# Performance work log

Hardware: AMD Instinct MI355X
Metric: run time of the kernel (lower is better)

## Reference

```python
import jax, jax.numpy as jnp
import numpy as np

EPS = 1e-12

def _l2norm(x):
    # F.normalize(p=2, dim=-1) semantics: x / max(||x||, eps)
    n = jnp.sqrt(jnp.sum(x * x, axis=-1, keepdims=True))
    return x / jnp.maximum(n, EPS)

def _split_heads(x, h):
    b, l, d = x.shape
    return x.reshape(b, l, h, d // h).transpose(0, 2, 1, 3)  # (B,H,L,dh)

def _join_heads(x):
    b, h, l, dh = x.shape
    return x.transpose(0, 2, 1, 3).reshape(b, l, h * dh)

def setup_inputs() -> dict:
    key = jax.random.key(0)
    B, L, D = 4, 4096, 1024
    ks = jax.random.split(key, 12)
    s = 1.0 / np.sqrt(D)
    inp = {
        "queries": jax.random.normal(ks[0], (B, L, D), jnp.float32),
        "values": jax.random.normal(ks[1], (B, L, D), jnp.float32),
        "keys": jax.random.normal(ks[2], (B, L, D), jnp.float32),
        "key_attention_mask": jnp.ones((B, L), jnp.float32),
        "Wq": jax.random.uniform(ks[3], (D, D), jnp.float32, -s, s),
        "bq": jax.random.uniform(ks[4], (D,), jnp.float32, -s, s),
        "Wk": jax.random.uniform(ks[5], (D, D), jnp.float32, -s, s),
        "bk": jax.random.uniform(ks[6], (D,), jnp.float32, -s, s),
        "Wv": jax.random.uniform(ks[7], (D, D), jnp.float32, -s, s),
        "bv": jax.random.uniform(ks[8], (D,), jnp.float32, -s, s),
        "Wo": jax.random.uniform(ks[9], (D, D), jnp.float32, -s, s),
        "bo": jax.random.uniform(ks[10], (D,), jnp.float32, -s, s),
    }
    return inp

def reference(queries, values, keys, key_attention_mask, Wq, bq, Wk, bk, Wv, bv, Wo, bo):
    nhead = 16
    L2 = keys.shape[1]
    qp = jnp.einsum('bld,ed->ble', queries, Wq) + bq
    kp = jnp.einsum('bld,ed->ble', keys, Wk) + bk
    vp = jnp.einsum('bld,ed->ble', values, Wv) + bv
    Q = _split_heads(qp, nhead)   # (B,H,L1,dh)
    K = _split_heads(kp, nhead)   # (B,H,L2,dh)
    V = _split_heads(vp, nhead)   # (B,H,L2,dh)
    V_minus = jnp.minimum(V, 0.0)
    V_plus = jnp.maximum(V, 0.0)
    Q = jax.nn.sigmoid(Q)
    scaled_K = jax.nn.sigmoid(K) / L2
    # AmplitudeEmbedding: L2-normalize feature maps along feature dim
    Q = _l2norm(Q)
    scaled_K = _l2norm(scaled_K)
    kv_plus = jnp.einsum('bhld,bhlc,bl->bhdc', scaled_K, V_plus, key_attention_mask)
    heads_plus = _l2norm(jnp.einsum('bhld,bhdc->bhlc', Q, kv_plus))
    kv_minus = jnp.einsum('bhld,bhlc,bl->bhdc', scaled_K, V_minus, key_attention_mask)
    heads_minus = _l2norm(jnp.einsum('bhld,bhdc->bhlc', Q, kv_minus))
    out = _join_heads(heads_plus + heads_minus)  # (B,L1,D)
    return jnp.einsum('blc,dc->bld', out, Wo) + bo
```

## Files before the change

### kernel.cpp

```cpp
#include <hip/hip_runtime.h>
#include <stdint.h>

#define B_  4
#define L_  4096
#define D_  1024
#define H_  16
#define DH  64
#define M_  (B_*L_)

typedef _Float16 f16;
typedef __attribute__((ext_vector_type(8))) _Float16 f16x8;
typedef __attribute__((ext_vector_type(4))) _Float16 f16x4;
typedef __attribute__((ext_vector_type(4))) float    f32x4;

__device__ __forceinline__ void cp16(const void* g, void* l) {
  __builtin_amdgcn_global_load_lds(
      (const __attribute__((address_space(1))) void*)g,
      (__attribute__((address_space(3))) void*)l,
      16, 0, 0);
}

#define MFMA(a,b,c) __builtin_amdgcn_mfma_f32_16x16x32_f16(a,b,c,0,0,0)

#define PH_IN do { __builtin_amdgcn_s_barrier(); \
  asm volatile("s_waitcnt lgkmcnt(0)" ::: "memory"); \
  __builtin_amdgcn_sched_barrier(0); \
  __builtin_amdgcn_s_setprio(1); } while (0)
#define PH_OUT do { __builtin_amdgcn_s_setprio(0); \
  __builtin_amdgcn_sched_barrier(0); \
  asm volatile("" ::: "memory"); \
  __builtin_amdgcn_s_barrier(); } while (0)
#define PH_OUT_VM(nimm) do { __builtin_amdgcn_s_setprio(0); \
  __builtin_amdgcn_sched_barrier(0); \
  asm volatile("s_waitcnt vmcnt(" #nimm ")" ::: "memory"); \
  __builtin_amdgcn_s_barrier(); } while (0)

__global__ __launch_bounds__(256) void k_cvt_f16(const float* __restrict__ x,
                                                 f16* __restrict__ y, int n8) {
  int i = blockIdx.x * 256 + threadIdx.x;
  if (i >= n8) return;
  const float4* xv = (const float4*)x;
  float4 a = xv[2*i], b = xv[2*i+1];
  f16x8 o;
  o[0]=(f16)a.x; o[1]=(f16)a.y; o[2]=(f16)a.z; o[3]=(f16)a.w;
  o[4]=(f16)b.x; o[5]=(f16)b.y; o[6]=(f16)b.z; o[7]=(f16)b.w;
  ((f16x8*)y)[i] = o;
}

__global__ __launch_bounds__(256) void k_cvt2(const float* __restrict__ x0,
                                              f16* __restrict__ y0,
                                              const float* __restrict__ x1,
                                              f16* __restrict__ y1, int n8each) {
  int i = blockIdx.x * 256 + threadIdx.x;
  const float* x = x0; f16* y = y0;
  if (i >= n8each) { x = x1; y = y1; i -= n8each; }
  const float4* xv = (const float4*)x;
  float4 a = xv[2*i], b = xv[2*i+1];
  f16x8 o;
  o[0]=(f16)a.x; o[1]=(f16)a.y; o[2]=(f16)a.z; o[3]=(f16)a.w;
  o[4]=(f16)b.x; o[5]=(f16)b.y; o[6]=(f16)b.z; o[7]=(f16)b.w;
  ((f16x8*)y)[i] = o;
}

__device__ __forceinline__ void split_one(const float* __restrict__ x,
                                          f16* __restrict__ cat, int i) {
  float4 a = ((const float4*)x)[i];
  int n  = i >> 8;
  int k4 = i & 255;
  f16 h0=(f16)a.x, h1=(f16)a.y, h2=(f16)a.z, h3=(f16)a.w;
  f16x4 hv = {h0, h1, h2, h3};
  f16x4 lv = {(f16)(a.x-(float)h0), (f16)(a.y-(float)h1),
              (f16)(a.z-(float)h2), (f16)(a.w-(float)h3)};
  size_t rh = (size_t)((n >> 4) * 32 + (n & 15));
  ((f16x4*)cat)[rh * 256 + k4]        = hv;
  ((f16x4*)cat)[(rh + 16) * 256 + k4] = lv;
}

__global__ __launch_bounds__(256) void k_split2(const float* __restrict__ x0,
                                                f16* __restrict__ c0,
                                                const float* __restrict__ x1,
                                                f16* __restrict__ c1, int n4each) {
  int i = blockIdx.x * 256 + threadIdx.x;
  if (i < n4each) split_one(x0, c0, i);
  else            split_one(x1, c1, i - n4each);
}

struct GemmJob {
  const f16* A; const f16* Bw; const float* bias; const float* mask;
  float* Cf; f16* Ch; int mode; int N;
};

__global__ __launch_bounds__(512, 1) void k_gemm8(GemmJob j0, GemmJob j1,
                                                  int nblk0, int M, int K) {
  __shared__ __align__(16) char smem[135168];
  char* sA = smem;
  char* sB = smem + 65536;
  const int t = threadIdx.x;

  int raw = (int)blockIdx.x;
  GemmJob J; int bid, nblk;
  if (raw < nblk0) { J = j0; bid = raw;         nblk = nblk0; }
  else             { J = j1; bid = raw - nblk0; nblk = (int)gridDim.x - nblk0; }
  const int N = J.N;
  const int nbn = N >> 8;
  {
    int cpx = nblk >> 3;
    bid = (bid & 7) * cpx + (bid >> 3);
  }
  const int bm = (bid / nbn) << 8;
  const int bn = (bid % nbn) << 8;
  const int lane = t & 63, wave = t >> 6;
  const int wm = wave >> 2;
  const int wn = wave & 3;
  const int fm = lane & 15, fkb = lane >> 4;

  const f16* Ab = J.A;
  const f16* Bb = J.Bw;
  auto SA_ = [&](int T, int buf, int half) {
#pragma unroll
    for (int q = 0; q < 2; ++q) {
      int li = (q << 9) + t;
      int row = li >> 3, cb = li & 7;
      const f16* g = Ab + (size_t)(bm + (half << 7) + row) * K
                        + (T << 6) + ((cb ^ (row & 7)) << 3);
      cp16(g, sA + buf * 32768 + half * 16384 + li * 16);
    }
  };
  auto SB_ = [&](int T, int buf, int half) {
#pragma unroll
    for (int q = 0; q < 2; ++q) {
      int li = (q << 9) + t;
      int row = li >> 3, cb = li & 7;
      const f16* g = Bb + (size_t)(bn + (half << 7) + row) * K
                        + (T << 6) + ((cb ^ (row & 7)) << 3);
      cp16(g, sB + buf * 32768 + half * 16384 + li * 16);
    }
  };
  auto LDA = [&](int buf, int i, int ks) -> f16x8 {
    int row = (i << 4) + fm;
    int blk = ((ks << 2) + fkb) ^ (row & 7);
    return *(const f16x8*)(sA + buf * 32768 + (wm << 14) + (row << 7) + (blk << 4));
  };
  auto LDB = [&](int buf, int j, int ks) -> f16x8 {
    int row = ((wn & 1) << 6) + (j << 4) + fm;
    int blk = ((ks << 2) + fkb) ^ (row & 7);
    return *(const f16x8*)(sB + buf * 32768 + ((wn >> 1) << 14) + (row << 7) + (blk << 4));
  };

  f32x4 acc[8][4] = {};

  SA_(0, 0, 0); SA_(0, 0, 1);
  SB_(0, 0, 0); SB_(0, 0, 1);
  SB_(1, 1, 0); SB_(1, 1, 1);
  asm volatile("s_waitcnt vmcnt(4)" ::: "memory");
  __builtin_amdgcn_s_barrier();

  const int NI = K >> 7;
  for (int it = 0; it < NI; ++it) {
    const bool nl = (it != NI - 1);
    const int t2 = 2 * it + 2, t3 = 2 * it + 3;
    f16x8 aL[4][2], aH[4][2], bA[2][2], bB[2][2];

#pragma unroll
    for (int i = 0; i < 4; ++i) { aL[i][0] = LDA(0,i,0); aL[i][1] = LDA(0,i,1); }
#pragma unroll
    for (int j = 0; j < 2; ++j) { bA[j][0] = LDB(0,j,0); bA[j][1] = LDB(0,j,1); }
    SA_(2*it+1, 1, 0);
    PH_IN;
#pragma unroll
    for (int i = 0; i < 4; ++i)
#pragma unroll
      for (int j = 0; j < 2; ++j) {
        acc[i][j] = MFMA(aL[i][0], bA[j][0], acc[i][j]);
        acc[i][j] = MFMA(aL[i][1], bA[j][1], acc[i][j]);
      }
    PH_OUT;
#pragma unroll
    for (int j = 0; j < 2; ++j) { bB[j][0] = LDB(0,j+2,0); bB[j][1] = LDB(0,j+2,1); }
    SA_(2*it+1, 1, 1);
    PH_IN;
#pragma unroll
    for (int i = 0; i < 4; ++i)
#pragma unroll
      for (int j = 0; j < 2; ++j) {
        acc[i][j+2] = MFMA(aL[i][0], bB[j][0], acc[i][j+2]);
        acc[i][j+2] = MFMA(aL[i][1], bB[j][1], acc[i][j+2]);
      }
    PH_OUT;
#pragma unroll
    for (int i = 0; i < 4; ++i) { aH[i][0] = LDA(0,i+4,0); aH[i][1] = LDA(0,i+4,1); }
    if (nl) SB_(t2, 0, 0);
    PH_IN;
#pragma unroll
    for (int i = 0; i < 4; ++i)
#pragma unroll
      for (int j = 0; j < 2; ++j) {
        acc[i+4][j] = MFMA(aH[i][0], bA[j][0], acc[i+4][j]);
        acc[i+4][j] = MFMA(aH[i][1], bA[j][1], acc[i+4][j]);
      }
    PH_OUT;
    if (nl) SB_(t2, 0, 1);
    PH_IN;
#pragma unroll
    for (int i = 0; i < 4; ++i)
#pragma unroll
      for (int j = 0; j < 2; ++j) {
        acc[i+4][j+2] = MFMA(aH[i][0], bB[j][0], acc[i+4][j+2]);
        acc[i+4][j+2] = MFMA(aH[i][1], bB[j][1], acc[i+4][j+2]);
      }
    if (nl) PH_OUT_VM(4); else PH_OUT_VM(0);
#pragma unroll
    for (int i = 0; i < 4; ++i) { aL[i][0] = LDA(1,i,0); aL[i][1] = LDA(1,i,1); }
#pragma unroll
    for (int j = 0; j < 2; ++j) { bA[j][0] = LDB(1,j,0); bA[j][1] = LDB(1,j,1); }
    if (nl) SA_(t2, 0, 0);
    PH_IN;
#pragma unroll
    for (int i = 0; i < 4; ++i)
#pragma unroll
      for (int j = 0; j < 2; ++j) {
        acc[i][j] = MFMA(aL[i][0], bA[j][0], acc[i][j]);
        acc[i][j] = MFMA(aL[i][1], bA[j][1], acc[i][j]);
      }
    PH_OUT;
#pragma unroll
    for (int j = 0; j < 2; ++j) { bB[j][0] = LDB(1,j+2,0); bB[j][1] = LDB(1,j+2,1); }
    if (nl) SA_(t2, 0, 1);
    PH_IN;
#pragma unroll
    for (int i = 0; i < 4; ++i)
#pragma unroll
      for (int j = 0; j < 2; ++j) {
        acc[i][j+2] = MFMA(aL[i][0], bB[j][0], acc[i][j+2]);
        acc[i][j+2] = MFMA(aL[i][1], bB[j][1], acc[i][j+2]);
      }
    PH_OUT;
#pragma unroll
    for (int i = 0; i < 4; ++i) { aH[i][0] = LDA(1,i+4,0); aH[i][1] = LDA(1,i+4,1); }
    if (nl) SB_(t3, 1, 0);
    PH_IN;
#pragma unroll
    for (int i = 0; i < 4; ++i)
#pragma unroll
      for (int j = 0; j < 2; ++j) {
        acc[i+4][j] = MFMA(aH[i][0], bA[j][0], acc[i+4][j]);
        acc[i+4][j] = MFMA(aH[i][1], bA[j][1], acc[i+4][j]);
      }
    PH_OUT;
    if (nl) SB_(t3, 1, 1);
    PH_IN;
#pragma unroll
    for (int i = 0; i < 4; ++i)
#pragma unroll
      for (int j = 0; j < 2; ++j) {
        acc[i+4][j+2] = MFMA(aH[i][0], bB[j][0], acc[i+4][j+2]);
        acc[i+4][j+2] = MFMA(aH[i][1], bB[j][1], acc[i+4][j+2]);
      }
    PH_OUT_VM(4);
  }

  const int cr = (lane >> 4) << 2, ccol = lane & 15;
  float* sOut = (float*)smem;
  if (J.mode == 1) {
    float bvj[4];
#pragma unroll
    for (int j = 0; j < 4; ++j) bvj[j] = J.bias[bn + wn*64 + j*16 + ccol];
    const int rbr = t >> 6;
    const int c4  = (t & 63) * 4;
    for (int h = 0; h < 2; ++h) {
      if (wm == h) {
#pragma unroll
        for (int i = 0; i < 8; ++i)
#pragma unroll
          for (int r = 0; r < 4; ++r) {
            int rl = i*16 + cr + r;
#pragma unroll
            for (int j = 0; j < 4; ++j)
              sOut[rl*260 + wn*64 + j*16 + ccol] = acc[i][j][r] + bvj[j];
          }
      }
      __syncthreads();
#pragma unroll
      for (int sp = 0; sp < 16; ++sp) {
        int rr = sp*8 + rbr;
        int gm = bm + h*128 + rr;
        f32x4 v = *(const f32x4*)&sOut[rr*260 + c4];
        float s0 = 1.0f / (1.0f + __expf(-v[0]));
        float s1 = 1.0f / (1.0f + __expf(-v[1]));
        float s2 = 1.0f / (1.0f + __expf(-v[2]));
        float s3 = 1.0f / (1.0f + __expf(-v[3]));
        float ss = s0*s0 + s1*s1 + s2*s2 + s3*s3;
        ss += __shfl_xor(ss, 1, 64);
        ss += __shfl_xor(ss, 2, 64);
        ss += __shfl_xor(ss, 4, 64);
        ss += __shfl_xor(ss, 8, 64);
        float sc = 1.0f / fmaxf(sqrtf(ss), 1e-12f);
        if (J.mask) sc *= J.mask[gm];
        f16x4 o = {(f16)(s0*sc), (f16)(s1*sc), (f16)(s2*sc), (f16)(s3*sc)};
        *(f16x4*)&J.Ch[(size_t)gm * N + bn + c4] = o;
      }
      __syncthreads();
    }
  } else {
#pragma unroll
    for (int j2 = 0; j2 < 2; ++j2) {
      int ocl = wn*32 + j2*16 + ccol;
      float bv = J.bias[(bn >> 1) + ocl];
#pragma unroll
      for (int i = 0; i < 8; ++i)
#pragma unroll
        for (int r = 0; r < 4; ++r) {
          int rl = wm*128 + i*16 + cr + r;
          sOut[rl*132 + ocl] = acc[i][2*j2][r] + acc[i][2*j2+1][r] + bv;
        }
    }
    __syncthreads();
    const int No = N >> 1;
#pragma unroll
    for (int sp = 0; sp < 16; ++sp) {
      int rl = sp*16 + (t >> 5);
      int c4 = (t & 31) * 4;
      f32x4 v = *(const f32x4*)&sOut[rl*132 + c4];
      size_t g = (size_t)(bm + rl) * No + (bn >> 1) + c4;
      if (J.mode == 2) {
        f16x4 o = {(f16)v[0], (f16)v[1], (f16)v[2], (f16)v[3]};
        *(f16x4*)&J.Ch[g] = o;
      } else {
        *(f32x4*)&J.Cf[g] = v;
      }
    }
  }
}

#define SKT 72
__global__ __launch_bounds__(256) void k_kv_mfma(const f16* __restrict__ Kh,
                                                 const f16* __restrict__ Vh,
                                                 float* __restrict__ part) {
  __shared__ __align__(16) f16 sKt[64 * SKT];
  __shared__ __align__(16) f16 sVt[128 * SKT];
  int head = blockIdx.x >> 3, chunk = blockIdx.x & 7;
  int b = head >> 4, h = head & 15;
  int t = threadIdx.x, lane = t & 63, wave = t >> 6;
  int lp = t & 31, g8 = (t >> 5) << 3;
  size_t rowbase = (size_t)b * L_ + (size_t)chunk * 512;
  const f16* Kb = Kh + rowbase * D_ + h * DH;
  const f16* Vb = Vh + rowbase * D_ + h * DH;

  const int fm = lane & 15, fk = (lane >> 4) << 3;
  const int wm2 = (wave & 1) * 2;
  const int wn4 = (wave >> 1) * 4;
  f32x4 acc[2][4] = {};

  for (int l0 = 0; l0 < 512; l0 += 64) {
    __syncthreads();
    {
      const f16* r0 = Kb + (size_t)(l0 + 2*lp) * D_ + g8;
      f16x8 a0 = *(const f16x8*)r0;
      f16x8 a1 = *(const f16x8*)(r0 + D_);
#pragma unroll
      for (int j = 0; j < 8; ++j) {
        union { f16 h2[2]; uint32_t u; } pk;
        pk.h2[0] = a0[j]; pk.h2[1] = a1[j];
        *(uint32_t*)&sKt[(g8 + j) * SKT + 2*lp] = pk.u;
      }
      const f16* v0p = Vb + (size_t)(l0 + 2*lp) * D_ + g8;
      f16x8 b0 = *(const f16x8*)v0p;
      f16x8 b1 = *(const f16x8*)(v0p + D_);
#pragma unroll
      for (int j = 0; j < 8; ++j) {
        float x0 = (float)b0[j], x1 = (float)b1[j];
        union { f16 h2[2]; uint32_t u; } pp, pm;
        pp.h2[0] = (f16)fmaxf(x0, 0.f); pp.h2[1] = (f16)fmaxf(x1, 0.f);
        pm.h2[0] = (f16)fminf(x0, 0.f); pm.h2[1] = (f16)fminf(x1, 0.f);
        *(uint32_t*)&sVt[(g8 + j) * SKT + 2*lp]        = pp.u;
        *(uint32_t*)&sVt[(64 + g8 + j) * SKT + 2*lp]   = pm.u;
      }
    }
    __syncthreads();
#pragma unroll
    for (int ks = 0; ks < 2; ++ks) {
      f16x8 af[2], bf[4];
#pragma unroll
      for (int i = 0; i < 2; ++i)
        af[i] = *(const f16x8*)&sKt[((wm2+i)*16 + fm) * SKT + ks*32 + fk];
#pragma unroll
      for (int j = 0; j < 4; ++j)
        bf[j] = *(const f16x8*)&sVt[((wn4+j)*16 + fm) * SKT + ks*32 + fk];
#pragma unroll
      for (int i = 0; i < 2; ++i)
#pragma unroll
        for (int j = 0; j < 4; ++j)
          acc[i][j] = MFMA(af[i], bf[j], acc[i][j]);
    }
  }
  const int cr = (lane >> 4) << 2, ccol = lane & 15;
  float* pb = part + (size_t)(head * 8 + chunk) * 8192;
#pragma unroll
  for (int i = 0; i < 2; ++i)
#pragma unroll
    for (int j = 0; j < 4; ++j) {
      int d = (wm2 + i) * 16 + cr;
      int c2 = (wn4 + j) * 16 + ccol;
#pragma unroll
      for (int r = 0; r < 4; ++r)
        pb[(d + r) * 128 + c2] = acc[i][j][r];
    }
}

__global__ __launch_bounds__(256) void k_kv_redcvt(const float* __restrict__ part,
                                                   f16* __restrict__ kvh) {
  int head = blockIdx.x, t = threadIdx.x;
  int c = t >> 1, half = t & 1;
  const float* src = part + (size_t)head * 8 * 8192 + half * 32 * 128 + c;
  f16* dst = kvh + (size_t)head * 8192 + c * 64 + half * 32;
  f16 buf[32];
#pragma unroll
  for (int kk = 0; kk < 32; ++kk) {
    float s = 0.f;
#pragma unroll
    for (int ch = 0; ch < 8; ++ch) s += src[(size_t)ch * 8192 + kk * 128];
    buf[kk] = (f16)s;
  }
#pragma unroll
  for (int q = 0; q < 4; ++q) ((f16x8*)dst)[q] = *(const f16x8*)&buf[q * 8];
}

#define SH 72
__global__ __launch_bounds__(256) void k_heads_mfma(const f16* __restrict__ Qh,
                                                    const f16* __restrict__ kvh,
                                                    f16* __restrict__ O) {
  __shared__ __align__(16) char hsmem[2 * 128 * SH * 2];
  f16* sQ  = (f16*)hsmem;
  f16* sKV = (f16*)(hsmem + 128 * SH * 2);
  int bi = blockIdx.x;
  int head = bi >> 5, mt = bi & 31;
  int b = head >> 4, h = head & 15;
  int t = threadIdx.x, lane = t & 63, wave = t >> 6;
  size_t qbase = ((size_t)(b * L_ + mt * 128)) * D_ + h * DH;
  const f16* kvp = kvh + (size_t)head * 8192;
#pragma unroll
  for (int p = 0; p < 4; ++p) {
    int c = p * 256 + t;
    int row = c >> 3, off = (c & 7) * 8;
    f16x8 q = *(const f16x8*)(Qh + qbase + (size_t)row * D_ + off);
    *(f16x8*)&sQ[row * SH + off] = q;
    f16x8 kv8 = *(const f16x8*)(kvp + row * 64 + off);
    *(f16x8*)&sKV[row * SH + off] = kv8;
  }
  __syncthreads();

  const int fm = lane & 15, fk = (lane >> 4) << 3;
  const int wm = wave * 32;
  f32x4 acc[2][8] = {};
#pragma unroll
  for (int ks = 0; ks < 2; ++ks) {
    f16x8 a0 = *(const f16x8*)&sQ[(wm + fm) * SH + ks * 32 + fk];
    f16x8 a1 = *(const f16x8*)&sQ[(wm + 16 + fm) * SH + ks * 32 + fk];
#pragma unroll
    for (int j = 0; j < 8; ++j) {
      f16x8 bj = *(const f16x8*)&sKV[(j * 16 + fm) * SH + ks * 32 + fk];
      acc[0][j] = MFMA(a0, bj, acc[0][j]);
      acc[1][j] = MFMA(a1, bj, acc[1][j]);
    }
  }
  __syncthreads();
  float* sOf = (float*)hsmem;
  const int cr = (lane >> 4) << 2, ccol = lane & 15;
#pragma unroll
  for (int i = 0; i < 2; ++i)
#pragma unroll
    for (int r = 0; r < 4; ++r) {
      int row = wm + i * 16 + cr + r;
      float sp = 0.f, sm = 0.f;
#pragma unroll
      for (int j = 0; j < 4; ++j) {
        sp += acc[i][j][r] * acc[i][j][r];
        sm += acc[i][j + 4][r] * acc[i][j + 4][r];
      }
      sp += __shfl_xor(sp, 1, 64); sm += __shfl_xor(sm, 1, 64);
      sp += __shfl_xor(sp, 2, 64); sm += __shfl_xor(sm, 2, 64);
      sp += __shfl_xor(sp, 4, 64); sm += __shfl_xor(sm, 4, 64);
      sp += __shfl_xor(sp, 8, 64); sm += __shfl_xor(sm, 8, 64);
      float rp = 1.0f / fmaxf(sqrtf(sp), 1e-12f);
      float rm = 1.0f / fmaxf(sqrtf(sm), 1e-12f);
#pragma unroll
      for (int j = 0; j < 4; ++j)
        sOf[row * 68 + j * 16 + ccol] = acc[i][j][r] * rp + acc[i][j + 4][r] * rm;
    }
  __syncthreads();
#pragma unroll
  for (int sp = 0; sp < 8; ++sp) {
    int rl = sp * 16 + (t >> 4);
    int c4 = (t & 15) * 4;
    f32x4 v = *(const f32x4*)&sOf[rl * 68 + c4];
    f16x4 o = {(f16)v[0], (f16)v[1], (f16)v[2], (f16)v[3]};
    *(f16x4*)&O[qbase + (size_t)rl * D_ + c4] = o;
  }
}

extern "C" void kernel_launch(void* const* d_in, const int* in_sizes, int n_in,
                              void* d_out, int out_size, void* d_ws, size_t ws_size,
                              hipStream_t stream) {
  const float* queries = (const float*)d_in[0];
  const float* values  = (const float*)d_in[1];
  const float* keys    = (const float*)d_in[2];
  const float* mask    = (const float*)d_in[3];
  const float* Wq = (const float*)d_in[4];  const float* bq = (const float*)d_in[5];
  const float* Wk = (const float*)d_in[6];  const float* bk = (const float*)d_in[7];
  const float* Wv = (const float*)d_in[8];  const float* bv = (const float*)d_in[9];
  const float* Wo = (const float*)d_in[10]; const float* bo = (const float*)d_in[11];
  float* out = (float*)d_out;

  const size_t MB = 1024ull * 1024ull;
  const size_t NEED = 160 * MB;
  if (ws_size < NEED) return;

  char* ws = (char*)d_ws;
  const size_t DD = (size_t)D_ * D_;
  f16*   Wqh  = (f16*)(ws);
  f16*   Wkh  = (f16*)(ws + 2 * MB);
  f16*   Wcv  = (f16*)(ws + 4 * MB);
  f16*   Wco  = (f16*)(ws + 8 * MB);
  f16*   Ah   = (f16*)(ws + 12 * MB);
  f16*   Qh   = (f16*)(ws + 44 * MB);
  f16*   kvh  = (f16*)(ws + 78 * MB);
  float* part = (float*)(ws + 80 * MB);
  f16*   kp   = (f16*)(ws + 96 * MB);
  f16*   vp   = (f16*)(ws + 128 * MB);

  const int DD8 = (int)(DD / 8);
  const int DD4 = (int)(DD / 4);
  const int n8  = M_ * D_ / 8;

  f16* q16 = Ah;
  f16* k16 = vp;
  f16* v16 = Ah;

  k_cvt2 <<<2 * DD8 / 256, 256, 0, stream>>>(Wq, Wqh, Wk, Wkh, DD8);
  k_split2<<<2 * DD4 / 256, 256, 0, stream>>>(Wv, Wcv, Wo, Wco, DD4);

  k_cvt2<<<2 * n8 / 256, 256, 0, stream>>>(queries, q16, keys, k16, n8);
  {
    GemmJob jq = { q16, Wqh, bq, nullptr, nullptr, Qh, 1, 1024 };
    GemmJob jk = { k16, Wkh, bk, mask,    nullptr, kp, 1, 1024 };
    k_gemm8<<<512, 512, 0, stream>>>(jq, jk, 256, M_, 1024);
  }

  k_cvt_f16<<<n8 / 256, 256, 0, stream>>>(values, v16, n8);
  {
    GemmJob jv = { v16, Wcv, bv, nullptr, nullptr, vp, 2, 2048 };
    k_gemm8<<<512, 512, 0, stream>>>(jv, jv, 512, M_, 1024);
  }

  k_kv_mfma<<<64 * 8, 256, 0, stream>>>(kp, vp, part);
  k_kv_redcvt<<<64, 256, 0, stream>>>(part, kvh);
  k_heads_mfma<<<64 * 32, 256, 0, stream>>>(Qh, kvh, Ah);

  {
    GemmJob jo = { Ah, Wco, bo, nullptr, out, nullptr, 3, 2048 };
    k_gemm8<<<512, 512, 0, stream>>>(jo, jo, 512, M_, 1024);
  }
}
```

Measured before the change: 508.9 us.

## Fuse fp32-to-fp16 activation conversion into GEMM A-tile loading

The GEMM now reads the fp32 activation A operand straight into registers, converts it to fp16 and stores it swizzled into LDS. This removes the separate conversion kernels for queries, keys and values and their fp16 round trip through memory. The heads kernel now writes fp32 output, which the output GEMM converts the same way. The cost is twice the A-operand global traffic per GEMM, extra VGPR pressure, and the loss of async global-to-LDS loads for A, which changes the waitcnt pipelining.

```diff
diff --git a/kernel.cpp b/kernel.cpp
--- a/kernel.cpp
+++ b/kernel.cpp
@@ -30,22 +30,7 @@
   __builtin_amdgcn_sched_barrier(0); \
   asm volatile("" ::: "memory"); \
   __builtin_amdgcn_s_barrier(); } while (0)
-#define PH_OUT_VM(nimm) do { __builtin_amdgcn_s_setprio(0); \
-  __builtin_amdgcn_sched_barrier(0); \
-  asm volatile("s_waitcnt vmcnt(" #nimm ")" ::: "memory"); \
-  __builtin_amdgcn_s_barrier(); } while (0)
-
-__global__ __launch_bounds__(256) void k_cvt_f16(const float* __restrict__ x,
-                                                 f16* __restrict__ y, int n8) {
-  int i = blockIdx.x * 256 + threadIdx.x;
-  if (i >= n8) return;
-  const float4* xv = (const float4*)x;
-  float4 a = xv[2*i], b = xv[2*i+1];
-  f16x8 o;
-  o[0]=(f16)a.x; o[1]=(f16)a.y; o[2]=(f16)a.z; o[3]=(f16)a.w;
-  o[4]=(f16)b.x; o[5]=(f16)b.y; o[6]=(f16)b.z; o[7]=(f16)b.w;
-  ((f16x8*)y)[i] = o;
-}
+#define VMW(nimm) asm volatile("s_waitcnt vmcnt(" #nimm ")" ::: "memory")
 
 __global__ __launch_bounds__(256) void k_cvt2(const float* __restrict__ x0,
                                               f16* __restrict__ y0,
@@ -86,7 +71,7 @@
 }
 
 struct GemmJob {
-  const f16* A; const f16* Bw; const float* bias; const float* mask;
+  const float* A; const f16* Bw; const float* bias; const float* mask;
   float* Cf; f16* Ch; int mode; int N;
 };
 
@@ -114,18 +99,28 @@
   const int wn = wave & 3;
   const int fm = lane & 15, fkb = lane >> 4;
 
-  const f16* Ab = J.A;
-  const f16* Bb = J.Bw;
-  auto SA_ = [&](int T, int buf, int half) {
-#pragma unroll
-    for (int q = 0; q < 2; ++q) {
-      int li = (q << 9) + t;
-      int row = li >> 3, cb = li & 7;
-      const f16* g = Ab + (size_t)(bm + (half << 7) + row) * K
-                        + (T << 6) + ((cb ^ (row & 7)) << 3);
-      cp16(g, sA + buf * 32768 + half * 16384 + li * 16);
-    }
-  };
+  const float* Af = J.A;
+  const f16*   Bb = J.Bw;
+
+#define AISS(RR, HALF, T_) do { \
+  _Pragma("unroll") for (int q = 0; q < 2; ++q) { \
+    int li = (q << 9) + t; int row = li >> 3, cb = li & 7; \
+    const float* gp = Af + (size_t)(bm + ((HALF) << 7) + row) * K \
+                         + ((T_) << 6) + (cb << 3); \
+    RR[2*q]   = *(const float4*)gp; \
+    RR[2*q+1] = *(const float4*)(gp + 4); \
+  } } while (0)
+
+#define ACVT(RR, HALF, BUF) do { \
+  _Pragma("unroll") for (int q = 0; q < 2; ++q) { \
+    int li = (q << 9) + t; int row = li >> 3, cb = li & 7; \
+    f16x8 o; \
+    o[0]=(f16)RR[2*q].x;   o[1]=(f16)RR[2*q].y;   o[2]=(f16)RR[2*q].z;   o[3]=(f16)RR[2*q].w; \
+    o[4]=(f16)RR[2*q+1].x; o[5]=(f16)RR[2*q+1].y; o[6]=(f16)RR[2*q+1].z; o[7]=(f16)RR[2*q+1].w; \
+    *(f16x8*)(sA + (BUF) * 32768 + (HALF) * 16384 \
+              + (((row << 3) + (cb ^ (row & 7))) << 4)) = o; \
+  } } while (0)
+
   auto SB_ = [&](int T, int buf, int half) {
 #pragma unroll
     for (int q = 0; q < 2; ++q) {
@@ -148,11 +143,15 @@
   };
 
   f32x4 acc[8][4] = {};
-
-  SA_(0, 0, 0); SA_(0, 0, 1);
+  float4 rA0[4], rA1[4];
+
+  AISS(rA0, 0, 0); AISS(rA1, 1, 0);
   SB_(0, 0, 0); SB_(0, 0, 1);
   SB_(1, 1, 0); SB_(1, 1, 1);
-  asm volatile("s_waitcnt vmcnt(4)" ::: "memory");
+  VMW(12); ACVT(rA0, 0, 0);
+  VMW(8);  ACVT(rA1, 1, 0);
+  VMW(4);
+  asm volatile("s_waitcnt lgkmcnt(0)" ::: "memory");
   __builtin_amdgcn_s_barrier();
 
   const int NI = K >> 7;
@@ -165,7 +164,7 @@
     for (int i = 0; i < 4; ++i) { aL[i][0] = LDA(0,i,0); aL[i][1] = LDA(0,i,1); }
 #pragma unroll
     for (int j = 0; j < 2; ++j) { bA[j][0] = LDB(0,j,0); bA[j][1] = LDB(0,j,1); }
-    SA_(2*it+1, 1, 0);
+    AISS(rA0, 0, 2*it+1);
     PH_IN;
 #pragma unroll
     for (int i = 0; i < 4; ++i)
@@ -177,7 +176,7 @@
     PH_OUT;
 #pragma unroll
     for (int j = 0; j < 2; ++j) { bB[j][0] = LDB(0,j+2,0); bB[j][1] = LDB(0,j+2,1); }
-    SA_(2*it+1, 1, 1);
+    AISS(rA1, 1, 2*it+1);
     PH_IN;
 #pragma unroll
     for (int i = 0; i < 4; ++i)
@@ -189,7 +188,8 @@
     PH_OUT;
 #pragma unroll
     for (int i = 0; i < 4; ++i) { aH[i][0] = LDA(0,i+4,0); aH[i][1] = LDA(0,i+4,1); }
-    if (nl) SB_(t2, 0, 0);
+    if (nl) { SB_(t2, 0, 0); VMW(6); } else { VMW(4); }
+    ACVT(rA0, 0, 1);
     PH_IN;
 #pragma unroll
     for (int i = 0; i < 4; ++i)
@@ -199,7 +199,8 @@
         acc[i+4][j] = MFMA(aH[i][1], bA[j][1], acc[i+4][j]);
       }
     PH_OUT;
-    if (nl) SB_(t2, 0, 1);
+    if (nl) { SB_(t2, 0, 1); VMW(4); } else { VMW(0); }
+    ACVT(rA1, 1, 1);
     PH_IN;
 #pragma unroll
     for (int i = 0; i < 4; ++i)
@@ -208,12 +209,12 @@
         acc[i+4][j+2] = MFMA(aH[i][0], bB[j][0], acc[i+4][j+2]);
         acc[i+4][j+2] = MFMA(aH[i][1], bB[j][1], acc[i+4][j+2]);
       }
-    if (nl) PH_OUT_VM(4); else PH_OUT_VM(0);
+    PH_OUT;
 #pragma unroll
     for (int i = 0; i < 4; ++i) { aL[i][0] = LDA(1,i,0); aL[i][1] = LDA(1,i,1); }
 #pragma unroll
     for (int j = 0; j < 2; ++j) { bA[j][0] = LDB(1,j,0); bA[j][1] = LDB(1,j,1); }
-    if (nl) SA_(t2, 0, 0);
+    if (nl) AISS(rA0, 0, t2);
     PH_IN;
 #pragma unroll
     for (int i = 0; i < 4; ++i)
@@ -225,7 +226,7 @@
     PH_OUT;
 #pragma unroll
     for (int j = 0; j < 2; ++j) { bB[j][0] = LDB(1,j+2,0); bB[j][1] = LDB(1,j+2,1); }
-    if (nl) SA_(t2, 0, 1);
+    if (nl) AISS(rA1, 1, t2);
     PH_IN;
 #pragma unroll
     for (int i = 0; i < 4; ++i)
@@ -237,7 +238,7 @@
     PH_OUT;
 #pragma unroll
     for (int i = 0; i < 4; ++i) { aH[i][0] = LDA(1,i+4,0); aH[i][1] = LDA(1,i+4,1); }
-    if (nl) SB_(t3, 1, 0);
+    if (nl) { SB_(t3, 1, 0); VMW(6); ACVT(rA0, 0, 0); }
     PH_IN;
 #pragma unroll
     for (int i = 0; i < 4; ++i)
@@ -247,7 +248,7 @@
         acc[i+4][j] = MFMA(aH[i][1], bA[j][1], acc[i+4][j]);
       }
     PH_OUT;
-    if (nl) SB_(t3, 1, 1);
+    if (nl) { SB_(t3, 1, 1); VMW(4); ACVT(rA1, 1, 0); }
     PH_IN;
 #pragma unroll
     for (int i = 0; i < 4; ++i)
@@ -256,7 +257,7 @@
         acc[i+4][j+2] = MFMA(aH[i][0], bB[j][0], acc[i+4][j+2]);
         acc[i+4][j+2] = MFMA(aH[i][1], bB[j][1], acc[i+4][j+2]);
       }
-    PH_OUT_VM(4);
+    PH_OUT;
   }
 
   const int cr = (lane >> 4) << 2, ccol = lane & 15;
@@ -330,6 +331,8 @@
       }
     }
   }
+#undef AISS
+#undef ACVT
 }
 
 #define SKT 72
@@ -428,7 +431,7 @@
 #define SH 72
 __global__ __launch_bounds__(256) void k_heads_mfma(const f16* __restrict__ Qh,
                                                     const f16* __restrict__ kvh,
-                                                    f16* __restrict__ O) {
+                                                    float* __restrict__ O) {
   __shared__ __align__(16) char hsmem[2 * 128 * SH * 2];
   f16* sQ  = (f16*)hsmem;
   f16* sKV = (f16*)(hsmem + 128 * SH * 2);
@@ -493,8 +496,7 @@
     int rl = sp * 16 + (t >> 4);
     int c4 = (t & 15) * 4;
     f32x4 v = *(const f32x4*)&sOf[rl * 68 + c4];
-    f16x4 o = {(f16)v[0], (f16)v[1], (f16)v[2], (f16)v[3]};
-    *(f16x4*)&O[qbase + (size_t)rl * D_ + c4] = o;
+    *(f32x4*)&O[qbase + (size_t)rl * D_ + c4] = v;
   }
 }
 
@@ -512,7 +514,7 @@
   float* out = (float*)d_out;
 
   const size_t MB = 1024ull * 1024ull;
-  const size_t NEED = 160 * MB;
+  const size_t NEED = 126 * MB;
   if (ws_size < NEED) return;
 
   char* ws = (char*)d_ws;
@@ -521,43 +523,36 @@
   f16*   Wkh  = (f16*)(ws + 2 * MB);
   f16*   Wcv  = (f16*)(ws + 4 * MB);
   f16*   Wco  = (f16*)(ws + 8 * MB);
-  f16*   Ah   = (f16*)(ws + 12 * MB);
-  f16*   Qh   = (f16*)(ws + 44 * MB);
-  f16*   kvh  = (f16*)(ws + 78 * MB);
-  float* part = (float*)(ws + 80 * MB);
-  f16*   kp   = (f16*)(ws + 96 * MB);
-  f16*   vp   = (f16*)(ws + 128 * MB);
+  f16*   Qh   = (f16*)(ws + 12 * MB);
+  f16*   kp   = (f16*)(ws + 44 * MB);
+  f16*   vp   = (f16*)(ws + 76 * MB);
+  float* part = (float*)(ws + 108 * MB);
+  f16*   kvh  = (f16*)(ws + 124 * MB);
+  float* Ao   = (float*)(ws + 44 * MB);
 
   const int DD8 = (int)(DD / 8);
   const int DD4 = (int)(DD / 4);
-  const int n8  = M_ * D_ / 8;
-
-  f16* q16 = Ah;
-  f16* k16 = vp;
-  f16* v16 = Ah;
 
   k_cvt2 <<<2 * DD8 / 256, 256, 0, stream>>>(Wq, Wqh, Wk, Wkh, DD8);
   k_split2<<<2 * DD4 / 256, 256, 0, stream>>>(Wv, Wcv, Wo, Wco, DD4);
 
-  k_cvt2<<<2 * n8 / 256, 256, 0, stream>>>(queries, q16, keys, k16, n8);
   {
-    GemmJob jq = { q16, Wqh, bq, nullptr, nullptr, Qh, 1, 1024 };
-    GemmJob jk = { k16, Wkh, bk, mask,    nullptr, kp, 1, 1024 };
+    GemmJob jq = { queries, Wqh, bq, nullptr, nullptr, Qh, 1, 1024 };
+    GemmJob jk = { keys,    Wkh, bk, mask,    nullptr, kp, 1, 1024 };
     k_gemm8<<<512, 512, 0, stream>>>(jq, jk, 256, M_, 1024);
   }
 
-  k_cvt_f16<<<n8 / 256, 256, 0, stream>>>(values, v16, n8);
   {
-    GemmJob jv = { v16, Wcv, bv, nullptr, nullptr, vp, 2, 2048 };
+    GemmJob jv = { values, Wcv, bv, nullptr, nullptr, vp, 2, 2048 };
     k_gemm8<<<512, 512, 0, stream>>>(jv, jv, 512, M_, 1024);
   }
 
   k_kv_mfma<<<64 * 8, 256, 0, stream>>>(kp, vp, part);
   k_kv_redcvt<<<64, 256, 0, stream>>>(part, kvh);
-  k_heads_mfma<<<64 * 32, 256, 0, stream>>>(Qh, kvh, Ah);
+  k_heads_mfma<<<64 * 32, 256, 0, stream>>>(Qh, kvh, Ao);
 
   {
-    GemmJob jo = { Ah, Wco, bo, nullptr, out, nullptr, 3, 2048 };
+    GemmJob jo = { Ao, Wco, bo, nullptr, out, nullptr, 3, 2048 };
     k_gemm8<<<512, 512, 0, stream>>>(jo, jo, 512, M_, 1024);
   }
 }
```

New measurement: 664.2 us. 1.31x slower.
